# Optimization experiments

Measured on AMD Instinct MI355X. Metric: run time of the kernel, lower is better.

## Reference

```python
import jax, jax.numpy as jnp
import numpy as np

K_SPLINE = 3
GRID_N = 3
NUM_BASIS = GRID_N + K_SPLINE  # 6 coefficients per spline edge


def _make_grid(in_dim):
    # pykan-style uniform grid on [-1, 1] extended by k knots each side
    h = 2.0 / GRID_N
    g = -1.0 + h * jnp.arange(-K_SPLINE, GRID_N + K_SPLINE + 1, dtype=jnp.float32)
    return jnp.broadcast_to(g, (in_dim, g.shape[0]))  # [in, G+2k+1]


def _b_splines(x, grid):
    # Cox-de Boor recursion. x: [N, in], grid: [in, G+2k+1] -> [N, in, G+k]
    x = x[:, :, None]
    g = grid[None, :, :]
    B = ((x >= g[:, :, :-1]) & (x < g[:, :, 1:])).astype(x.dtype)
    for p in range(1, K_SPLINE + 1):
        B = ((x - g[:, :, :-(p + 1)]) / (g[:, :, p:-1] - g[:, :, :-(p + 1)]) * B[:, :, :-1]
             + (g[:, :, p + 1:] - x) / (g[:, :, p + 1:] - g[:, :, 1:-p]) * B[:, :, 1:])
    return B


def _kan_layer(x, grid, coef, scale_base, scale_sp, bias):
    # KANLayer: out_j = sum_i scale_base[i,j]*silu(x_i) + scale_sp[i,j]*spline_ij(x_i) + bias_j
    B = _b_splines(x, grid)                              # [N, in, G+k]
    spline = jnp.einsum('nib,iob->nio', B, coef)         # [N, in, out]
    act = scale_base[None] * jax.nn.silu(x)[:, :, None] + scale_sp[None] * spline
    return act.sum(axis=1) + bias[None, :]


def _calculate_w(strain, params):
    # strain: [B, S, 3] -> W: [B, S, 1]
    s1, s2, s3 = strain[..., 0], strain[..., 1], strain[..., 2]
    # C = 2E + I with E = [[s1, s3/2], [s3/2, s2]]
    a = 2.0 * s1 + 1.0
    d = 2.0 * s2 + 1.0
    b = s3
    detC = a * d - b * b
    logJ = 0.5 * jnp.log(detC)                           # log(det(C)**0.5)
    # analytic eigvalsh of symmetric 2x2, ascending order; double-where keeps
    # gradients finite at the degenerate point (strain == 0, C == I)
    m = 0.5 * (a + d)
    h2 = 0.25 * (a - d) ** 2 + b * b
    r = jnp.where(h2 > 0, jnp.sqrt(jnp.where(h2 > 0, h2, 1.0)), 0.0)
    eigs = jnp.sqrt(jnp.stack([m - r, m + r], axis=-1))  # principal stretches [B,S,2]
    aux = detC ** (-1.0 / 6.0)                           # J**(-1/3)
    reg = eigs * aux[..., None]
    kan_in = jnp.concatenate([reg ** params['ki0'],
                              (logJ * params['ki1'])[..., None]], axis=-1)  # [B,S,3]
    Bn, Sn = kan_in.shape[0], kan_in.shape[1]
    flat = kan_in.reshape(Bn * Sn, 3)
    h = _kan_layer(flat, _make_grid(3), params['coef0'], params['sb0'], params['sp0'], params['b0'])
    out = _kan_layer(h, _make_grid(1), params['coef1'], params['sb1'], params['sp1'], params['b1'])
    return out.reshape(Bn, Sn, -1)


def _forward(strain, params):
    # grad of sum(W) wrt strain (grad_outputs = ones), minus the same grad at zero strain.
    gradW = jax.grad(lambda s: _calculate_w(s, params).sum())(strain)
    zeros = jnp.zeros((1, 1, 3), strain.dtype)           # grad at 0 is identical per element
    grad0 = jax.grad(lambda s: _calculate_w(s, params).sum())(zeros)
    return gradW - grad0


def setup_inputs() -> dict:
    key = jax.random.key(0)
    ks = jax.random.split(key, 4)
    B, S = 4096, 512
    strain = 0.1 * jax.random.uniform(ks[0], (B, S, 3), dtype=jnp.float32)
    coef0 = 0.1 * jax.random.normal(ks[1], (3, 1, NUM_BASIS), dtype=jnp.float32)
    coef1 = 0.1 * jax.random.normal(ks[2], (1, 1, NUM_BASIS), dtype=jnp.float32)
    return {
        'strain': strain,
        'coef0': coef0,
        'sb0': jnp.full((3, 1), 1.0 / np.sqrt(3.0), jnp.float32),
        'sp0': jnp.ones((3, 1), jnp.float32),
        'b0': jnp.zeros((1,), jnp.float32),
        'coef1': coef1,
        'sb1': jnp.ones((1, 1), jnp.float32),
        'sp1': jnp.ones((1, 1), jnp.float32),
        'b1': jnp.zeros((1,), jnp.float32),
        'ki0': jnp.asarray(1.37, jnp.float32),  # ki[0] = 1 + random()
        'ki1': jnp.asarray(1.0, jnp.float32),   # ki[-1] fixed to 1.0 in __init__
    }


def reference(strain, coef0, sb0, sp0, b0, coef1, sb1, sp1, b1, ki0, ki1):
    params = {'coef0': coef0, 'sb0': sb0, 'sp0': sp0, 'b0': b0,
              'coef1': coef1, 'sb1': sb1, 'sp1': sp1, 'b1': b1,
              'ki0': ki0, 'ki1': ki1}
    return _forward(strain, params)
```

## Files before the change

### kernel.cpp

```cpp
#include <hip/hip_runtime.h>
#include <math.h>

#define NB 6

struct Params {
    float sb0[3], sp0[3];
    float b0;
    float sb1, sp1;
    float k3, k6, kh;
    float cL;
    float ch;
};

__device__ __forceinline__ float fexp2(float x) { return __builtin_amdgcn_exp2f(x); }
__device__ __forceinline__ float flog2(float x) { return __builtin_amdgcn_logf(x); }
__device__ __forceinline__ float frcp(float x)  { return __builtin_amdgcn_rcpf(x); }
__device__ __forceinline__ float frsq(float x)  { return __builtin_amdgcn_rsqf(x); }

__device__ __forceinline__ void spline_eval(float x, const float4* __restrict__ tab,
                                            float& sp, float& dsp) {
    float u  = fmaf(x, 1.5f, 4.5f);
    float fi = floorf(u);
    float f  = u - fi;
    int   i  = (int)fi;
    bool  in = (u >= 0.0f && u < 9.0f);
    float msk  = in ? 1.0f : 0.0f;
    float msk15 = in ? 1.5f : 0.0f;
    i = i < 0 ? 0 : (i > 8 ? 8 : i);
    const float4 A = tab[i];
    sp  = msk  * fmaf(fmaf(fmaf(A.w, f, A.z), f, A.y), f, A.x);
    float a2z = A.z + A.z;
    float f3  = 3.0f * f;
    dsp = msk15 * fmaf(f, fmaf(f3, A.w, a2z), A.y);
}

__device__ __forceinline__ void silu_fd(float x, float& s, float& ds) {
    float e   = fexp2(-1.44269504f * x);
    float sig = frcp(1.0f + e);
    s  = x * sig;
    ds = sig * fmaf(x, 1.0f - sig, 1.0f);
}

__device__ void grad_sample(float s1, float s2, float s3, const Params& P,
                            const float4 (*__restrict__ tab)[9], float g[3]) {
    float q   = s1 - s2;
    float m   = s1 + s2 + 1.0f;
    float b   = s3;
    float h2  = fmaf(q, q, b * b);
    float irr = h2 > 0.0f ? frsq(h2) : 0.0f;
    float r   = h2 * irr;
    float t1  = m - r, t2 = m + r;
    float invDet = frcp(t1 * t2);
    float invt1 = t2 * invDet, invt2 = t1 * invDet;
    float Lt1 = flog2(t1), Lt2 = flog2(t2);
    float x0  = fexp2(fmaf(Lt1, P.k3, -Lt2 * P.k6));
    float x1  = fexp2(fmaf(Lt2, P.k3, -Lt1 * P.k6));
    float x2  = (Lt1 + Lt2) * P.cL;

    float xs[3] = {x0, x1, x2};
    float hacc  = P.b0;
    float gx[3];
#pragma unroll
    for (int i = 0; i < 3; ++i) {
        float sp, dsp;
        spline_eval(xs[i], tab[i], sp, dsp);
        float si, dsi; silu_fd(xs[i], si, dsi);
        hacc += P.sb0[i] * si + P.sp0[i] * sp;
        gx[i] = P.sb0[i] * dsi + P.sp0[i] * dsp;
    }
    float sp2, dsp2;
    spline_eval(hacc, tab[3], sp2, dsp2);
    float si2, dsi2; silu_fd(hacc, si2, dsi2);
    float dWdh = P.sb1 * dsi2 + P.sp1 * dsp2;

    float P0 = dWdh * gx[0] * x0;
    float P1 = dWdh * gx[1] * x1;
    float w2c = dWdh * gx[2];
    float A = P.kh * P0 * invt1;
    float B = P.kh * P1 * invt2;
    float C = invDet * fmaf(-P.k6, P0 + P1, P.ch * w2c);
    float u0 = (B - A) * irr;
    float w  = fmaf(C, m, 0.5f * (A + B));
    float t  = q * fmaf(0.5f, u0, -C);
    g[0] = 2.0f * (w + t);
    g[1] = 2.0f * (w - t);
    g[2] = b * fmaf(-2.0f, C, u0);
}

__global__ __launch_bounds__(256) void kan_grad(
        const float* __restrict__ strain, float* __restrict__ out, int n,
        const float* __restrict__ c0, const float* __restrict__ sb0,
        const float* __restrict__ sp0, const float* __restrict__ b0,
        const float* __restrict__ c1, const float* __restrict__ sb1,
        const float* __restrict__ sp1, const float* __restrict__ ki0,
        const float* __restrict__ ki1) {
    __shared__ float4 tab[4][9];
    __shared__ float g0s[3];

    const int t = threadIdx.x;
    if (t < 36) {
        int tbl = t / 9, cell = t % 9;
        const float* cp = (tbl < 3) ? (c0 + tbl * NB) : c1;
        float cv[4];
#pragma unroll
        for (int kk = 0; kk < 4; ++kk) {
            int j = cell + kk - 3;
            cv[kk] = (j >= 0 && j < NB) ? cp[j] : 0.0f;
        }
        const float c16 = 1.0f / 6.0f;
        float a0 = (cv[0] + 4.0f * cv[1] + cv[2]) * c16;
        float a1 = (cv[2] - cv[0]) * 0.5f;
        float a2 = (cv[0] - 2.0f * cv[1] + cv[2]) * 0.5f;
        float a3 = (cv[3] - cv[0] + 3.0f * (cv[1] - cv[2])) * c16;
        tab[tbl][cell] = make_float4(a0, a1, a2, a3);
    }

    Params P;
#pragma unroll
    for (int i = 0; i < 3; ++i) { P.sb0[i] = sb0[i]; P.sp0[i] = sp0[i]; }
    P.b0 = b0[0];
    P.sb1 = sb1[0]; P.sp1 = sp1[0];
    float k = ki0[0], l = ki1[0];
    P.k3 = k * (1.0f / 3.0f);
    P.k6 = k * (1.0f / 6.0f);
    P.kh = k * 0.5f;
    P.cL = l * 0.34657359f;
    P.ch = l * 0.5f;

    __syncthreads();
    if (t == 0) {
        float g0[3];
        grad_sample(0.0f, 0.0f, 0.0f, P, tab, g0);
        g0s[0] = g0[0]; g0s[1] = g0[1]; g0s[2] = g0[2];
    }
    __syncthreads();
    const float g00 = g0s[0], g01 = g0s[1], g02 = g0s[2];

    const int ngroups = (n + 7) >> 3;
    for (int gi = blockIdx.x * blockDim.x + threadIdx.x; gi < ngroups;
         gi += gridDim.x * blockDim.x) {
        int i0 = gi * 8;
        if (i0 + 8 <= n) {
            const float4* sp4 = reinterpret_cast<const float4*>(strain + (size_t)i0 * 3);
            float4 v[6];
#pragma unroll
            for (int kk = 0; kk < 6; ++kk) v[kk] = sp4[kk];
            const float* in = reinterpret_cast<const float*>(v);
            float o[24];
#pragma unroll
            for (int kk = 0; kk < 8; ++kk) {
                float g[3];
                grad_sample(in[3 * kk], in[3 * kk + 1], in[3 * kk + 2], P, tab, g);
                o[3 * kk]     = g[0] - g00;
                o[3 * kk + 1] = g[1] - g01;
                o[3 * kk + 2] = g[2] - g02;
            }
            float4* op4 = reinterpret_cast<float4*>(out + (size_t)i0 * 3);
            const float4* ov = reinterpret_cast<const float4*>(o);
#pragma unroll
            for (int kk = 0; kk < 6; ++kk) op4[kk] = ov[kk];
        } else {
            for (int i = i0; i < n; ++i) {
                float g[3];
                grad_sample(strain[3 * i], strain[3 * i + 1], strain[3 * i + 2], P,
                            tab, g);
                out[3 * i]     = g[0] - g00;
                out[3 * i + 1] = g[1] - g01;
                out[3 * i + 2] = g[2] - g02;
            }
        }
    }
}

extern "C" void kernel_launch(void* const* d_in, const int* in_sizes, int n_in,
                              void* d_out, int out_size, void* d_ws, size_t ws_size,
                              hipStream_t stream) {
    const float* strain = (const float*)d_in[0];
    const float* c0  = (const float*)d_in[1];
    const float* sb0 = (const float*)d_in[2];
    const float* sp0 = (const float*)d_in[3];
    const float* b0  = (const float*)d_in[4];
    const float* c1  = (const float*)d_in[5];
    const float* sb1 = (const float*)d_in[6];
    const float* sp1 = (const float*)d_in[7];
    const float* ki0 = (const float*)d_in[9];
    const float* ki1 = (const float*)d_in[10];

    int n = in_sizes[0] / 3;
    int ngroups = (n + 7) / 8;
    int block = 256;
    int grid = (ngroups + block - 1) / block;
    if (grid > 8192) grid = 8192;

    kan_grad<<<grid, block, 0, stream>>>(strain, (float*)d_out, n,
                                         c0, sb0, sp0, b0, c1, sb1, sp1, ki0, ki1);
}
```

Baseline: 21.30 us.

## Stage strain chunks through shared memory for coalesced loads and stores

Each block now loads a 1024-sample chunk of strain into LDS with fully coalesced float4 reads. Each thread computes 4 samples from LDS, writes the results back to LDS, and the block then stores them to global memory coalesced. This replaces the earlier pattern where each thread read and wrote 96 contiguous bytes, which gives strided per-lane accesses. In exchange it adds 12 KB of LDS per block and three barriers per chunk, halves per-thread ILP (4 samples instead of 8), and the 12-float-stride LDS accesses may cause bank conflicts.

Result: no change. 21.70 us (+1.9%).

```diff
diff --git a/kernel.cpp b/kernel.cpp
--- a/kernel.cpp
+++ b/kernel.cpp
@@ -24,7 +24,7 @@
     float f  = u - fi;
     int   i  = (int)fi;
     bool  in = (u >= 0.0f && u < 9.0f);
-    float msk  = in ? 1.0f : 0.0f;
+    float msk   = in ? 1.0f : 0.0f;
     float msk15 = in ? 1.5f : 0.0f;
     i = i < 0 ? 0 : (i > 8 ? 8 : i);
     const float4 A = tab[i];
@@ -87,6 +87,9 @@
     g[2] = b * fmaf(-2.0f, C, u0);
 }
 
+#define CHUNK 1024
+#define CHUNK_F4 768
+
 __global__ __launch_bounds__(256) void kan_grad(
         const float* __restrict__ strain, float* __restrict__ out, int n,
         const float* __restrict__ c0, const float* __restrict__ sb0,
@@ -96,6 +99,7 @@
         const float* __restrict__ ki1) {
     __shared__ float4 tab[4][9];
     __shared__ float g0s[3];
+    __shared__ float buf[CHUNK * 3];
 
     const int t = threadIdx.x;
     if (t < 36) {
@@ -136,31 +140,42 @@
     __syncthreads();
     const float g00 = g0s[0], g01 = g0s[1], g02 = g0s[2];
 
-    const int ngroups = (n + 7) >> 3;
-    for (int gi = blockIdx.x * blockDim.x + threadIdx.x; gi < ngroups;
-         gi += gridDim.x * blockDim.x) {
-        int i0 = gi * 8;
-        if (i0 + 8 <= n) {
-            const float4* sp4 = reinterpret_cast<const float4*>(strain + (size_t)i0 * 3);
-            float4 v[6];
-#pragma unroll
-            for (int kk = 0; kk < 6; ++kk) v[kk] = sp4[kk];
-            const float* in = reinterpret_cast<const float*>(v);
-            float o[24];
-#pragma unroll
-            for (int kk = 0; kk < 8; ++kk) {
+    const int nchunks = (n + CHUNK - 1) / CHUNK;
+    for (int ch = blockIdx.x; ch < nchunks; ch += gridDim.x) {
+        size_t s0 = (size_t)ch * CHUNK;
+        int cnt = n - (int)s0; if (cnt > CHUNK) cnt = CHUNK;
+        if (cnt == CHUNK) {
+            const float4* g4 = reinterpret_cast<const float4*>(strain + s0 * 3);
+            float4* b4 = reinterpret_cast<float4*>(buf);
+            b4[t]       = g4[t];
+            b4[t + 256] = g4[t + 256];
+            b4[t + 512] = g4[t + 512];
+            __syncthreads();
+            float4* mine = reinterpret_cast<float4*>(buf + t * 12);
+            float4 i0v = mine[0], i1v = mine[1], i2v = mine[2];
+            float in[12] = { i0v.x, i0v.y, i0v.z, i0v.w,
+                             i1v.x, i1v.y, i1v.z, i1v.w,
+                             i2v.x, i2v.y, i2v.z, i2v.w };
+            float o[12];
+#pragma unroll
+            for (int kk = 0; kk < 4; ++kk) {
                 float g[3];
                 grad_sample(in[3 * kk], in[3 * kk + 1], in[3 * kk + 2], P, tab, g);
                 o[3 * kk]     = g[0] - g00;
                 o[3 * kk + 1] = g[1] - g01;
                 o[3 * kk + 2] = g[2] - g02;
             }
-            float4* op4 = reinterpret_cast<float4*>(out + (size_t)i0 * 3);
-            const float4* ov = reinterpret_cast<const float4*>(o);
-#pragma unroll
-            for (int kk = 0; kk < 6; ++kk) op4[kk] = ov[kk];
+            mine[0] = make_float4(o[0], o[1], o[2],  o[3]);
+            mine[1] = make_float4(o[4], o[5], o[6],  o[7]);
+            mine[2] = make_float4(o[8], o[9], o[10], o[11]);
+            __syncthreads();
+            float4* o4 = reinterpret_cast<float4*>(out + s0 * 3);
+            o4[t]       = b4[t];
+            o4[t + 256] = b4[t + 256];
+            o4[t + 512] = b4[t + 512];
+            __syncthreads();
         } else {
-            for (int i = i0; i < n; ++i) {
+            for (int i = (int)s0 + t; i < n; i += 256) {
                 float g[3];
                 grad_sample(strain[3 * i], strain[3 * i + 1], strain[3 * i + 2], P,
                             tab, g);
@@ -168,6 +183,7 @@
                 out[3 * i + 1] = g[1] - g01;
                 out[3 * i + 2] = g[2] - g02;
             }
+            __syncthreads();
         }
     }
 }
@@ -187,11 +203,9 @@
     const float* ki1 = (const float*)d_in[10];
 
     int n = in_sizes[0] / 3;
-    int ngroups = (n + 7) / 8;
-    int block = 256;
-    int grid = (ngroups + block - 1) / block;
-    if (grid > 8192) grid = 8192;
-
-    kan_grad<<<grid, block, 0, stream>>>(strain, (float*)d_out, n,
-                                         c0, sb0, sp0, b0, c1, sb1, sp1, ki0, ki1);
-}
+    int nchunks = (n + CHUNK - 1) / CHUNK;
+    int grid = nchunks < 8192 ? nchunks : 8192;
+
+    kan_grad<<<grid, 256, 0, stream>>>(strain, (float*)d_out, n,
+                                       c0, sb0, sp0, b0, c1, sb1, sp1, ki0, ki1);
+}
```

## Fold spline scales into padded derivative tables and compute reference gradient analytically

Applied to the files above, without the earlier changes.

Spline coefficient tables are padded to 12 cells so the in-range mask and floor disappear, and they are pre-scaled by sp0/sp1. Precomputed derivative polynomials are stored alongside them. The second-layer spline and silu values are dropped because only their derivatives are needed. The strain-zero reference gradient is now derived in closed form per thread instead of by a serial thread-0 evaluation with an extra barrier, and each thread handles 4 samples instead of 8. This trades more shared-memory loads and higher thread count for less ALU work and register pressure.

After: 19.21 us (median of 2 runs). 9.8% less time.

```diff
diff --git a/kernel.cpp b/kernel.cpp
--- a/kernel.cpp
+++ b/kernel.cpp
@@ -4,9 +4,8 @@
 #define NB 6
 
 struct Params {
-    float sb0[3], sp0[3];
-    float b0;
-    float sb1, sp1;
+    float sb0_0, sb0_1, sb0_2;
+    float b0, sb1;
     float k3, k6, kh;
     float cL;
     float ch;
@@ -17,32 +16,40 @@
 __device__ __forceinline__ float frcp(float x)  { return __builtin_amdgcn_rcpf(x); }
 __device__ __forceinline__ float frsq(float x)  { return __builtin_amdgcn_rsqf(x); }
 
-__device__ __forceinline__ void spline_eval(float x, const float4* __restrict__ tab,
-                                            float& sp, float& dsp) {
-    float u  = fmaf(x, 1.5f, 4.5f);
-    float fi = floorf(u);
-    float f  = u - fi;
-    int   i  = (int)fi;
-    bool  in = (u >= 0.0f && u < 9.0f);
-    float msk  = in ? 1.0f : 0.0f;
-    float msk15 = in ? 1.5f : 0.0f;
-    i = i < 0 ? 0 : (i > 8 ? 8 : i);
-    const float4 A = tab[i];
-    sp  = msk  * fmaf(fmaf(fmaf(A.w, f, A.z), f, A.y), f, A.x);
-    float a2z = A.z + A.z;
-    float f3  = 3.0f * f;
-    dsp = msk15 * fmaf(f, fmaf(f3, A.w, a2z), A.y);
+__device__ __forceinline__ void spline_sd(float x, const float4* __restrict__ t4,
+                                          float& sp, float& dsp) {
+    float u = fmaf(x, 1.5f, 5.5f);
+    int   i = (int)u;
+    i = i < 0 ? 0 : (i > 11 ? 11 : i);
+    float f = u - (float)i;
+    float4 A = t4[2 * i];
+    float4 B = t4[2 * i + 1];
+    sp  = fmaf(fmaf(fmaf(A.w, f, A.z), f, A.y), f, A.x);
+    dsp = fmaf(fmaf(B.z, f, B.y), f, B.x);
+}
+
+__device__ __forceinline__ float spline_d(float x, const float4* __restrict__ t4) {
+    float u = fmaf(x, 1.5f, 5.5f);
+    int   i = (int)u;
+    i = i < 0 ? 0 : (i > 11 ? 11 : i);
+    float f = u - (float)i;
+    float4 B = t4[2 * i + 1];
+    return fmaf(fmaf(B.z, f, B.y), f, B.x);
 }
 
 __device__ __forceinline__ void silu_fd(float x, float& s, float& ds) {
-    float e   = fexp2(-1.44269504f * x);
-    float sig = frcp(1.0f + e);
+    float sig = frcp(1.0f + fexp2(-1.44269504f * x));
     s  = x * sig;
     ds = sig * fmaf(x, 1.0f - sig, 1.0f);
 }
 
-__device__ void grad_sample(float s1, float s2, float s3, const Params& P,
-                            const float4 (*__restrict__ tab)[9], float g[3]) {
+__device__ __forceinline__ float silu_d(float x) {
+    float sig = frcp(1.0f + fexp2(-1.44269504f * x));
+    return sig * fmaf(x, 1.0f - sig, 1.0f);
+}
+
+__device__ __forceinline__ void grad_sample(float s1, float s2, float s3,
+        const Params& P, const float4* __restrict__ tb, float g[3]) {
     float q   = s1 - s2;
     float m   = s1 + s2 + 1.0f;
     float b   = s3;
@@ -57,25 +64,25 @@
     float x1  = fexp2(fmaf(Lt2, P.k3, -Lt1 * P.k6));
     float x2  = (Lt1 + Lt2) * P.cL;
 
-    float xs[3] = {x0, x1, x2};
-    float hacc  = P.b0;
-    float gx[3];
-#pragma unroll
-    for (int i = 0; i < 3; ++i) {
-        float sp, dsp;
-        spline_eval(xs[i], tab[i], sp, dsp);
-        float si, dsi; silu_fd(xs[i], si, dsi);
-        hacc += P.sb0[i] * si + P.sp0[i] * sp;
-        gx[i] = P.sb0[i] * dsi + P.sp0[i] * dsp;
-    }
-    float sp2, dsp2;
-    spline_eval(hacc, tab[3], sp2, dsp2);
-    float si2, dsi2; silu_fd(hacc, si2, dsi2);
-    float dWdh = P.sb1 * dsi2 + P.sp1 * dsp2;
-
-    float P0 = dWdh * gx[0] * x0;
-    float P1 = dWdh * gx[1] * x1;
-    float w2c = dWdh * gx[2];
+    float S0, D0, S1v, D1, S2v, D2;
+    spline_sd(x0, tb,      S0,  D0);
+    spline_sd(x1, tb + 24, S1v, D1);
+    spline_sd(x2, tb + 48, S2v, D2);
+    float si0, dsi0, si1, dsi1, si2, dsi2;
+    silu_fd(x0, si0, dsi0);
+    silu_fd(x1, si1, dsi1);
+    silu_fd(x2, si2, dsi2);
+    float hacc = P.b0 + fmaf(P.sb0_0, si0, S0) + fmaf(P.sb0_1, si1, S1v)
+               + fmaf(P.sb0_2, si2, S2v);
+    float gx0 = fmaf(P.sb0_0, dsi0, D0);
+    float gx1 = fmaf(P.sb0_1, dsi1, D1);
+    float gx2 = fmaf(P.sb0_2, dsi2, D2);
+
+    float dWdh = fmaf(P.sb1, silu_d(hacc), spline_d(hacc, tb + 72));
+
+    float P0  = dWdh * gx0 * x0;
+    float P1  = dWdh * gx1 * x1;
+    float w2c = dWdh * gx2;
     float A = P.kh * P0 * invt1;
     float B = P.kh * P1 * invt2;
     float C = invDet * fmaf(-P.k6, P0 + P1, P.ch * w2c);
@@ -94,32 +101,13 @@
         const float* __restrict__ c1, const float* __restrict__ sb1,
         const float* __restrict__ sp1, const float* __restrict__ ki0,
         const float* __restrict__ ki1) {
-    __shared__ float4 tab[4][9];
-    __shared__ float g0s[3];
+    __shared__ float4 tab4[96];
 
     const int t = threadIdx.x;
-    if (t < 36) {
-        int tbl = t / 9, cell = t % 9;
-        const float* cp = (tbl < 3) ? (c0 + tbl * NB) : c1;
-        float cv[4];
-#pragma unroll
-        for (int kk = 0; kk < 4; ++kk) {
-            int j = cell + kk - 3;
-            cv[kk] = (j >= 0 && j < NB) ? cp[j] : 0.0f;
-        }
-        const float c16 = 1.0f / 6.0f;
-        float a0 = (cv[0] + 4.0f * cv[1] + cv[2]) * c16;
-        float a1 = (cv[2] - cv[0]) * 0.5f;
-        float a2 = (cv[0] - 2.0f * cv[1] + cv[2]) * 0.5f;
-        float a3 = (cv[3] - cv[0] + 3.0f * (cv[1] - cv[2])) * c16;
-        tab[tbl][cell] = make_float4(a0, a1, a2, a3);
-    }
 
     Params P;
-#pragma unroll
-    for (int i = 0; i < 3; ++i) { P.sb0[i] = sb0[i]; P.sp0[i] = sp0[i]; }
-    P.b0 = b0[0];
-    P.sb1 = sb1[0]; P.sp1 = sp1[0];
+    P.sb0_0 = sb0[0]; P.sb0_1 = sb0[1]; P.sb0_2 = sb0[2];
+    P.b0 = b0[0]; P.sb1 = sb1[0];
     float k = ki0[0], l = ki1[0];
     P.k3 = k * (1.0f / 3.0f);
     P.k6 = k * (1.0f / 6.0f);
@@ -127,46 +115,76 @@
     P.cL = l * 0.34657359f;
     P.ch = l * 0.5f;
 
-    __syncthreads();
-    if (t == 0) {
-        float g0[3];
-        grad_sample(0.0f, 0.0f, 0.0f, P, tab, g0);
-        g0s[0] = g0[0]; g0s[1] = g0[1]; g0s[2] = g0[2];
+    if (t < 48) {
+        int tbl = t / 12, cell = t % 12;
+        float scale = (tbl < 3) ? sp0[tbl] : sp1[0];
+        const float* cp = (tbl < 3) ? (c0 + tbl * NB) : c1;
+        int  c    = cell - 1;
+        bool real = (cell >= 1 && cell <= 9);
+        float cv[4];
+#pragma unroll
+        for (int kk = 0; kk < 4; ++kk) {
+            int j = c + kk - 3;
+            cv[kk] = (real && j >= 0 && j < NB) ? cp[j] : 0.0f;
+        }
+        const float c16 = 1.0f / 6.0f;
+        float a0 = (cv[0] + 4.0f * cv[1] + cv[2]) * c16 * scale;
+        float a1 = (cv[2] - cv[0]) * 0.5f * scale;
+        float a2 = (cv[0] - 2.0f * cv[1] + cv[2]) * 0.5f * scale;
+        float a3 = (cv[3] - cv[0] + 3.0f * (cv[1] - cv[2])) * c16 * scale;
+        tab4[2 * t]     = make_float4(a0, a1, a2, a3);
+        tab4[2 * t + 1] = make_float4(1.5f * a1, 3.0f * a2, 4.5f * a3, 0.0f);
     }
     __syncthreads();
-    const float g00 = g0s[0], g01 = g0s[1], g02 = g0s[2];
-
-    const int ngroups = (n + 7) >> 3;
-    for (int gi = blockIdx.x * blockDim.x + threadIdx.x; gi < ngroups;
+
+    const float SI1 = 0.73105858f, DSI1 = 0.92767051f;
+    float S0g = tab4[2 * 7].x,        D0g = tab4[2 * 7 + 1].x;
+    float S1g = tab4[2 * 19].x,       D1g = tab4[2 * 19 + 1].x;
+    float4 A2 = tab4[2 * 29],         B2  = tab4[2 * 29 + 1];
+    const float fh = 0.5f;
+    float S2g = fmaf(fmaf(fmaf(A2.w, fh, A2.z), fh, A2.y), fh, A2.x);
+    float D2g = fmaf(fmaf(B2.z, fh, B2.y), fh, B2.x);
+    float hacc0 = P.b0 + fmaf(P.sb0_0, SI1, S0g) + fmaf(P.sb0_1, SI1, S1g) + S2g;
+    float gx0g = fmaf(P.sb0_0, DSI1, D0g);
+    float gx1g = fmaf(P.sb0_1, DSI1, D1g);
+    float gx2g = fmaf(P.sb0_2, 0.5f, D2g);
+    float dW0 = fmaf(P.sb1, silu_d(hacc0), spline_d(hacc0, tab4 + 72));
+    float P0g = dW0 * gx0g, P1g = dW0 * gx1g, w2g = dW0 * gx2g;
+    float Ag = P.kh * P0g, Bg = P.kh * P1g;
+    float Cg = fmaf(-P.k6, P0g + P1g, P.ch * w2g);
+    const float G = (Ag + Bg) + 2.0f * Cg;
+
+    const int ngroups = (n + 3) >> 2;
+    for (int gi = blockIdx.x * blockDim.x + t; gi < ngroups;
          gi += gridDim.x * blockDim.x) {
-        int i0 = gi * 8;
-        if (i0 + 8 <= n) {
+        int i0 = gi * 4;
+        if (i0 + 4 <= n) {
             const float4* sp4 = reinterpret_cast<const float4*>(strain + (size_t)i0 * 3);
-            float4 v[6];
+            float4 v0 = sp4[0], v1 = sp4[1], v2 = sp4[2];
+            float in[12] = { v0.x, v0.y, v0.z, v0.w,
+                             v1.x, v1.y, v1.z, v1.w,
+                             v2.x, v2.y, v2.z, v2.w };
+            float o[12];
 #pragma unroll
-            for (int kk = 0; kk < 6; ++kk) v[kk] = sp4[kk];
-            const float* in = reinterpret_cast<const float*>(v);
-            float o[24];
-#pragma unroll
-            for (int kk = 0; kk < 8; ++kk) {
+            for (int kk = 0; kk < 4; ++kk) {
                 float g[3];
-                grad_sample(in[3 * kk], in[3 * kk + 1], in[3 * kk + 2], P, tab, g);
-                o[3 * kk]     = g[0] - g00;
-                o[3 * kk + 1] = g[1] - g01;
-                o[3 * kk + 2] = g[2] - g02;
+                grad_sample(in[3 * kk], in[3 * kk + 1], in[3 * kk + 2], P, tab4, g);
+                o[3 * kk]     = g[0] - G;
+                o[3 * kk + 1] = g[1] - G;
+                o[3 * kk + 2] = g[2];
             }
             float4* op4 = reinterpret_cast<float4*>(out + (size_t)i0 * 3);
-            const float4* ov = reinterpret_cast<const float4*>(o);
-#pragma unroll
-            for (int kk = 0; kk < 6; ++kk) op4[kk] = ov[kk];
+            op4[0] = make_float4(o[0], o[1], o[2],  o[3]);
+            op4[1] = make_float4(o[4], o[5], o[6],  o[7]);
+            op4[2] = make_float4(o[8], o[9], o[10], o[11]);
         } else {
             for (int i = i0; i < n; ++i) {
                 float g[3];
                 grad_sample(strain[3 * i], strain[3 * i + 1], strain[3 * i + 2], P,
-                            tab, g);
-                out[3 * i]     = g[0] - g00;
-                out[3 * i + 1] = g[1] - g01;
-                out[3 * i + 2] = g[2] - g02;
+                            tab4, g);
+                out[3 * i]     = g[0] - G;
+                out[3 * i + 1] = g[1] - G;
+                out[3 * i + 2] = g[2];
             }
         }
     }
@@ -187,7 +205,7 @@
     const float* ki1 = (const float*)d_in[10];
 
     int n = in_sizes[0] / 3;
-    int ngroups = (n + 7) / 8;
+    int ngroups = (n + 3) / 4;
     int block = 256;
     int grid = (ngroups + block - 1) / block;
     if (grid > 8192) grid = 8192;
```
